# Kernel tuning notes

Measured on AMD Instinct MI355X. Metric: run time of the kernel, lower is better.

## Reference

```python
import jax, jax.numpy as jnp
import numpy as np

N_NODES = 100000
EMBED_DIM = 256


def _sage_conv(x, src, dst, W_l, b_l, W_r, num_nodes):
    # PyG SAGEConv (mean aggr): out = lin_l(mean_{j in N(i)} x_j) + lin_r(x_i)
    msg = x[src]                                              # [E, D] gather
    agg = jax.ops.segment_sum(msg, dst, num_segments=num_nodes)   # [N, D]
    cnt = jax.ops.segment_sum(jnp.ones((src.shape[0], 1), x.dtype), dst,
                              num_segments=num_nodes)         # [N, 1]
    mean = agg / jnp.maximum(cnt, 1.0)
    return mean @ W_l + b_l + x @ W_r


def setup_inputs() -> dict:
    key = jax.random.key(0)
    ks = jax.random.split(key, 12)
    D = EMBED_DIM
    glorot = 1.0 / np.sqrt(D)
    inp = {
        "emb": jax.random.uniform(ks[0], (N_NODES + 1, D), jnp.float32, 0.001, 0.3),
        "W1l": jax.random.uniform(ks[1], (D, D), jnp.float32, -glorot, glorot),
        "b1l": jnp.zeros((D,), jnp.float32),
        "W1r": jax.random.uniform(ks[2], (D, D), jnp.float32, -glorot, glorot),
        "W2l": jax.random.uniform(ks[3], (D, D), jnp.float32, -glorot, glorot),
        "b2l": jnp.zeros((D,), jnp.float32),
        "W2r": jax.random.uniform(ks[4], (D, D), jnp.float32, -glorot, glorot),
        "x_idx": jax.random.randint(ks[5], (N_NODES,), 0, N_NODES + 1, jnp.int64 if jax.config.read('jax_enable_x64') else jnp.int32),
        "edge_index": jax.random.randint(ks[6], (2, 1600000), 0, N_NODES, jnp.int32),
        "drugNodes": jax.random.randint(ks[7], (1024,), 0, N_NODES, jnp.int32),
        "seNodes": jax.random.randint(ks[8], (1024,), 0, N_NODES, jnp.int32),
    }
    return inp


def reference(emb, W1l, b1l, W1r, W2l, b2l, W2r, x_idx, edge_index, drugNodes, seNodes):
    src, dst = edge_index[0], edge_index[1]
    x = emb[x_idx]                                            # embedding lookup [N, D]
    x = _sage_conv(x, src, dst, W1l, b1l, W1r, x.shape[0])
    x = _sage_conv(x, src, dst, W2l, b2l, W2r, x.shape[0])
    drugEmbedding = x[drugNodes]
    seEmbedding = x[seNodes]
    return (drugEmbedding, seEmbedding, x)
```

## Files before the change

kernel.cpp:

```cpp
#include <hip/hip_runtime.h>
#include <hip/hip_bf16.h>


typedef __bf16 bf16x8 __attribute__((ext_vector_type(8)));
typedef __bf16 bf16x4 __attribute__((ext_vector_type(4)));
typedef float  f32x4  __attribute__((ext_vector_type(4)));
typedef float  f32x8  __attribute__((ext_vector_type(8)));

#define ROWB 1024
#define NPART 256
#define MAXBUK 2048

__device__ __forceinline__ void async_copy16(void* lds_dst, const void* g_src) {
  __builtin_amdgcn_global_load_lds(
      (const __attribute__((address_space(1))) void*)g_src,
      (__attribute__((address_space(3))) void*)lds_dst, 16, 0, 0);
}


__global__ void bin_count(const int* __restrict__ dst, int* __restrict__ hmat,
                          int E, int chunk, int nbuk) {
  __shared__ int lh[MAXBUK];
  int p = blockIdx.x, tid = threadIdx.x;
  for (int i = tid; i < nbuk; i += 256) lh[i] = 0;
  __syncthreads();
  int base = p * chunk, end = min(base + chunk, E);
  for (int e = base + tid; e < end; e += 256) atomicAdd(&lh[dst[e] >> 6], 1);
  __syncthreads();
  for (int i = tid; i < nbuk; i += 256) hmat[p * nbuk + i] = lh[i];
}

__global__ void col_scan(int* __restrict__ hmat, int* __restrict__ btot, int nbuk) {
  __shared__ int s[NPART];
  int b = blockIdx.x, t = threadIdx.x;
  int v = hmat[t * nbuk + b];
  s[t] = v; __syncthreads();
  for (int d = 1; d < NPART; d <<= 1) {
    int add = (t >= d) ? s[t - d] : 0;
    __syncthreads();
    s[t] += add;
    __syncthreads();
  }
  hmat[t * nbuk + b] = s[t] - v;
  if (t == NPART - 1) btot[b] = s[t];
}

__global__ void bucket_scan(const int* __restrict__ btot, int* __restrict__ boff, int nb) {
  __shared__ int s[2048];
  int t = threadIdx.x;
  for (int i = t; i < 2048; i += 1024) s[i] = (i < nb) ? btot[i] : 0;
  __syncthreads();
  for (int d = 1; d < 2048; d <<= 1) {
    int v0 = (t >= d) ? s[t - d] : 0;
    int v1 = (t + 1024 >= d) ? s[t + 1024 - d] : 0;
    __syncthreads();
    s[t] += v0; s[t + 1024] += v1;
    __syncthreads();
  }
  for (int i = t; i < nb; i += 1024) boff[i] = s[i] - btot[i];
}

__global__ void part_write(const int* __restrict__ src, const int* __restrict__ dst,
                           const int* __restrict__ hmat, const int* __restrict__ boff,
                           int* __restrict__ ebuf, int E, int chunk, int nbuk) {
  __shared__ int cur[MAXBUK];
  int p = blockIdx.x, tid = threadIdx.x;
  for (int i = tid; i < nbuk; i += 256) cur[i] = hmat[p * nbuk + i] + boff[i];
  __syncthreads();
  int base = p * chunk, end = min(base + chunk, E);
  for (int e = base + tid; e < end; e += 256) {
    int d = dst[e];
    int pos = atomicAdd(&cur[d >> 6], 1);
    ebuf[pos] = src[e] | ((d & 63) << 18);
  }
}

__global__ void node_hist(const int* __restrict__ ebuf, const int* __restrict__ boff,
                          const int* __restrict__ btot, int* __restrict__ cnt, int N) {
  __shared__ int lh[64];
  int b = blockIdx.x, tid = threadIdx.x;
  if (tid < 64) lh[tid] = 0;
  __syncthreads();
  int s0 = boff[b], s1 = s0 + btot[b];
  for (int i = s0 + tid; i < s1; i += 256) atomicAdd(&lh[ebuf[i] >> 18], 1);
  __syncthreads();
  int node = b * 64 + tid;
  if (tid < 64 && node < N) cnt[node] = lh[tid];
}

__global__ void scan_block_sums(const int* __restrict__ cnt, int* __restrict__ bsum, int n) {
  __shared__ int s[256];
  int i = blockIdx.x * 256 + threadIdx.x;
  s[threadIdx.x] = (i < n) ? cnt[i] : 0;
  __syncthreads();
  for (int d = 128; d > 0; d >>= 1) {
    if (threadIdx.x < d) s[threadIdx.x] += s[threadIdx.x + d];
    __syncthreads();
  }
  if (threadIdx.x == 0) bsum[blockIdx.x] = s[0];
}

__global__ void scan_tops(const int* __restrict__ bsum, int* __restrict__ bbase, int nb) {
  __shared__ int s[512];
  int t = threadIdx.x;
  int v = (t < nb) ? bsum[t] : 0;
  s[t] = v; __syncthreads();
  for (int d = 1; d < 512; d <<= 1) {
    int add = (t >= d) ? s[t - d] : 0;
    __syncthreads();
    s[t] += add;
    __syncthreads();
  }
  if (t < nb) bbase[t] = s[t] - v;
}

__global__ void scan_final(const int* __restrict__ cnt, const int* __restrict__ bbase,
                           int* __restrict__ offs, int n) {
  __shared__ int s[256];
  int t = threadIdx.x, i = blockIdx.x * 256 + t;
  int v = (i < n) ? cnt[i] : 0;
  s[t] = v; __syncthreads();
  for (int d = 1; d < 256; d <<= 1) {
    int add = (t >= d) ? s[t - d] : 0;
    __syncthreads();
    s[t] += add;
    __syncthreads();
  }
  if (i < n) offs[i] = bbase[blockIdx.x] + s[t] - v;
}

__global__ void csr_write(const int* __restrict__ ebuf, const int* __restrict__ boff,
                          const int* __restrict__ btot, const int* __restrict__ offs,
                          int* __restrict__ csr, int N) {
  __shared__ int cur[64];
  int b = blockIdx.x, tid = threadIdx.x;
  int node = b * 64 + tid;
  if (tid < 64) cur[tid] = (node < N) ? offs[node] : 0;
  __syncthreads();
  int s0 = boff[b], s1 = s0 + btot[b];
  for (int i = s0 + tid; i < s1; i += 256) {
    int e = ebuf[i];
    int p = atomicAdd(&cur[e >> 18], 1);
    csr[p] = e & 0x3FFFF;
  }
}


__global__ void prep_w_kernel(const float* __restrict__ W1l, const float* __restrict__ W1r,
                              const float* __restrict__ W2l, const float* __restrict__ W2r,
                              __bf16* __restrict__ Wt1, __bf16* __restrict__ Wt2) {
  int idx = blockIdx.x * 256 + threadIdx.x;
  int which = idx >> 17;
  int j = idx & 131071;
  int n = j >> 9, k = j & 511;
  const float* Wl = which ? W2l : W1l;
  const float* Wr = which ? W2r : W1r;
  float v = (k < 256) ? Wl[k * 256 + n] : Wr[(k - 256) * 256 + n];
  (which ? Wt2 : Wt1)[j] = (__bf16)v;
}

__global__ void gather_x_kernel(const float* __restrict__ emb, const int* __restrict__ x_idx,
                                char* __restrict__ xbase, int N) {
  int wave = threadIdx.x >> 6, lane = threadIdx.x & 63;
  int i = blockIdx.x * 4 + wave;
  if (i >= N) return;
  int s = x_idx[i];
  float4 v = *(const float4*)(emb + (size_t)s * 256 + lane * 4);
  bf16x4 o = { (__bf16)v.x, (__bf16)v.y, (__bf16)v.z, (__bf16)v.w };
  *(bf16x4*)(xbase + (size_t)i * ROWB + lane * 8) = o;
}


__global__ void sage_agg(const char* __restrict__ srcbase,
                         char* __restrict__ dstbase,
                         const int* __restrict__ csr, const int* __restrict__ cnt,
                         const int* __restrict__ offs, int N) {
  int wave = threadIdx.x >> 6, lane = threadIdx.x & 63;
  int i = blockIdx.x * 4 + wave;
  if (i >= N) return;
  int deg = cnt[i];
  const int* lp = csr + offs[i];
  int half = lane >> 5, l5 = lane & 31;
  const char* sb = srcbase + l5 * 16;

  f32x8 acc = (f32x8)0.f;

  int g8 = deg >> 3;
  for (int t = 0; t < g8; ++t) {
    const int* p = lp + t * 8 + half;
    int s0 = p[0], s1 = p[2], s2 = p[4], s3 = p[6];
    bf16x8 v0 = *(const bf16x8*)(sb + (size_t)s0 * ROWB);
    bf16x8 v1 = *(const bf16x8*)(sb + (size_t)s1 * ROWB);
    bf16x8 v2 = *(const bf16x8*)(sb + (size_t)s2 * ROWB);
    bf16x8 v3 = *(const bf16x8*)(sb + (size_t)s3 * ROWB);
#pragma unroll
    for (int k = 0; k < 8; ++k)
      acc[k] += ((float)v0[k] + (float)v1[k]) + ((float)v2[k] + (float)v3[k]);
  }

  int base = g8 * 8;
  int rem = deg & 7;
  int rp = rem >> 1;
  for (int u = 0; u < rp; ++u) {
    int s0 = lp[base + 2 * u + half];
    bf16x8 v0 = *(const bf16x8*)(sb + (size_t)s0 * ROWB);
#pragma unroll
    for (int k = 0; k < 8; ++k) acc[k] += (float)v0[k];
  }
  if ((rem & 1) && half == 0) {
    int s0 = lp[deg - 1];
    bf16x8 v0 = *(const bf16x8*)(sb + (size_t)s0 * ROWB);
#pragma unroll
    for (int k = 0; k < 8; ++k) acc[k] += (float)v0[k];
  }

  float inv = 1.0f / (float)(deg > 0 ? deg : 1);
  bf16x8 o;
#pragma unroll
  for (int k = 0; k < 8; ++k) {
    float s = acc[k] + __shfl_down(acc[k], 32);
    o[k] = (__bf16)(s * inv);
  }
  if (half == 0)
    *(bf16x8*)(dstbase + (size_t)i * ROWB + l5 * 16) = o;
}


template <int OUT_F32>
__global__ __launch_bounds__(256) void gemm_sage(const char* __restrict__ Abase,
                                                 const __bf16* __restrict__ Wt,
                                                 const float* __restrict__ bias,
                                                 char* __restrict__ outbase, int M) {
  __shared__ __align__(16) char lds[40960];
  const int tid = threadIdx.x;
  const int wave = tid >> 6, lane = tid & 63;
  const int r = lane & 15, q = lane >> 4;
  const int wm = wave >> 1, wn = wave & 1;
  const int row0 = blockIdx.x * 64;

  f32x4 acc[2][8];
#pragma unroll
  for (int t = 0; t < 2; ++t)
#pragma unroll
    for (int u = 0; u < 8; ++u) acc[t][u] = (f32x4)0.f;

  auto stage = [&](int kk, int buf) {
    char* lbase = lds + buf * 20480;
    int rowA = row0 + wave * 16 + r;
    rowA = rowA < M ? rowA : M - 1;
    async_copy16(lbase + wave * 1024 + lane * 16,
                 Abase + (size_t)rowA * ROWB + (size_t)(kk * 32 + q * 8) * 2);
#pragma unroll
    for (int i = 0; i < 4; ++i) {
      int h = wave * 4 + i;
      async_copy16(lbase + 4096 + h * 1024 + lane * 16,
                   (const char*)Wt + ((size_t)(h * 16 + r) * 512 + kk * 32 + q * 8) * 2);
    }
  };

  stage(0, 0);
  for (int kk = 0; kk < 16; ++kk) {
    __syncthreads();
    if (kk < 15) stage(kk + 1, (kk + 1) & 1);
    const char* lbase = lds + (kk & 1) * 20480;
    bf16x8 a0 = *(const bf16x8*)(lbase + (wm * 2 + 0) * 1024 + lane * 16);
    bf16x8 a1 = *(const bf16x8*)(lbase + (wm * 2 + 1) * 1024 + lane * 16);
#pragma unroll
    for (int u = 0; u < 8; ++u) {
      bf16x8 b = *(const bf16x8*)(lbase + 4096 + (wn * 8 + u) * 1024 + lane * 16);
      acc[0][u] = __builtin_amdgcn_mfma_f32_16x16x32_bf16(a0, b, acc[0][u], 0, 0, 0);
      acc[1][u] = __builtin_amdgcn_mfma_f32_16x16x32_bf16(a1, b, acc[1][u], 0, 0, 0);
    }
  }

#pragma unroll
  for (int t = 0; t < 2; ++t) {
    int rbase = row0 + wm * 32 + t * 16 + q * 4;
#pragma unroll
    for (int u = 0; u < 8; ++u) {
      int col = wn * 128 + u * 16 + r;
      float bv = bias[col];
#pragma unroll
      for (int j = 0; j < 4; ++j) {
        int row = rbase + j;
        if (row < M) {
          float v = acc[t][u][j] + bv;
          if (OUT_F32)
            *(float*)(outbase + (size_t)row * ROWB + col * 4) = v;
          else
            *(__bf16*)(outbase + (size_t)row * ROWB + 512 + col * 2) = (__bf16)v;
        }
      }
    }
  }
}


__global__ void gather_out_kernel(const float* __restrict__ x2, const int* __restrict__ drug,
                                  const int* __restrict__ se, float* __restrict__ out,
                                  int nd, int ns) {
  int wave = threadIdx.x >> 6, lane = threadIdx.x & 63;
  int ro = blockIdx.x * 4 + wave;
  if (ro >= nd + ns) return;
  int node = (ro < nd) ? drug[ro] : se[ro - nd];
  float4 v = *(const float4*)(x2 + (size_t)node * 256 + lane * 4);
  *(float4*)(out + (size_t)ro * 256 + lane * 4) = v;
}


extern "C" void kernel_launch(void* const* d_in, const int* in_sizes, int n_in,
                              void* d_out, int out_size, void* d_ws, size_t ws_size,
                              hipStream_t stream) {
  const float* emb  = (const float*)d_in[0];
  const float* W1l  = (const float*)d_in[1];
  const float* b1l  = (const float*)d_in[2];
  const float* W1r  = (const float*)d_in[3];
  const float* W2l  = (const float*)d_in[4];
  const float* b2l  = (const float*)d_in[5];
  const float* W2r  = (const float*)d_in[6];
  const int* x_idx  = (const int*)d_in[7];
  const int* edge   = (const int*)d_in[8];
  const int* drug   = (const int*)d_in[9];
  const int* se     = (const int*)d_in[10];

  const int N = in_sizes[7];
  const int E = in_sizes[8] / 2;
  const int nd = in_sizes[9], ns = in_sizes[10];
  const int* esrc = edge;
  const int* edst = edge + E;
  const int NBUK = (N + 63) >> 6;
  const int chunk = (E + NPART - 1) / NPART;

  char* ws = (char*)d_ws;
  size_t off = 0;
  char* xA1 = ws;                       off += (size_t)((N + 127) & ~127) * ROWB;
  __bf16* Wt1 = (__bf16*)(ws + off);    off += 512 * 256 * 2;
  __bf16* Wt2 = (__bf16*)(ws + off);    off += 512 * 256 * 2;
  int* cnt  = (int*)(ws + off);         off += ((size_t)N * 4 + 255) & ~(size_t)255;
  int* offs = (int*)(ws + off);         off += ((size_t)N * 4 + 255) & ~(size_t)255;
  int* csr  = (int*)(ws + off);         off += ((size_t)E * 4 + 255) & ~(size_t)255;
  int* bsum = (int*)(ws + off);         off += 4096;
  int* bbase = (int*)(ws + off);        off += 4096;
  int* ebuf = (int*)xA1;
  int* hmat = (int*)(xA1 + (8u << 20));
  int* btot = (int*)(xA1 + (16u << 20));
  int* boff = (int*)(xA1 + (16u << 20) + 16384);

  float* outp = (float*)d_out;
  float* x2 = outp + (size_t)(nd + ns) * 256;
  char* scratch2 = (char*)x2;

  const int NB = (N + 255) / 256;
  const int QB = (N + 3) / 4;
  const int GB = (N + 63) / 64;

  prep_w_kernel<<<(2 * 131072) / 256, 256, 0, stream>>>(W1l, W1r, W2l, W2r, Wt1, Wt2);

  bin_count<<<NPART, 256, 0, stream>>>(edst, hmat, E, chunk, NBUK);
  col_scan<<<NBUK, NPART, 0, stream>>>(hmat, btot, NBUK);
  bucket_scan<<<1, 1024, 0, stream>>>(btot, boff, NBUK);
  part_write<<<NPART, 256, 0, stream>>>(esrc, edst, hmat, boff, ebuf, E, chunk, NBUK);
  node_hist<<<NBUK, 256, 0, stream>>>(ebuf, boff, btot, cnt, N);
  scan_block_sums<<<NB, 256, 0, stream>>>(cnt, bsum, N);
  scan_tops<<<1, 512, 0, stream>>>(bsum, bbase, NB);
  scan_final<<<NB, 256, 0, stream>>>(cnt, bbase, offs, N);
  csr_write<<<NBUK, 256, 0, stream>>>(ebuf, boff, btot, offs, csr, N);

  gather_x_kernel<<<QB, 256, 0, stream>>>(emb, x_idx, xA1 + 512, N);
  sage_agg<<<QB, 256, 0, stream>>>(xA1 + 512, xA1, csr, cnt, offs, N);
  gemm_sage<0><<<GB, 256, 0, stream>>>(xA1, Wt1, b1l, scratch2, N);
  sage_agg<<<QB, 256, 0, stream>>>(scratch2 + 512, scratch2, csr, cnt, offs, N);
  gemm_sage<1><<<GB, 256, 0, stream>>>(scratch2, Wt2, b2l, scratch2, N);

  gather_out_kernel<<<(nd + ns + 3) / 4, 256, 0, stream>>>(x2, drug, se, outp, nd, ns);
}
```

Before: 679.6 us.

## Fuse neighbor mean aggregation into SAGE GEMM and collapse CSR offset scan

Adds a 512-thread fused kernel that computes the mean-aggregated neighbor rows for a 64-row tile directly into swizzled LDS, then runs the MFMA GEMM over both the mean and self halves without writing the mean back to global memory. Separately, the three-kernel global prefix scan for CSR offsets is replaced by a per-bucket wavefront shuffle scan inside the histogram kernel, using the already known bucket offsets. The fused path needs a second full-size workspace buffer and only runs when the workspace is large enough. The gather phase now runs with only 64 rows per block, so the gather and GEMM phases no longer overlap across kernels and occupancy is lower due to large LDS use.

```diff
diff --git a/kernel.cpp b/kernel.cpp
--- a/kernel.cpp
+++ b/kernel.cpp
@@ -75,8 +75,9 @@
   }
 }
 
-__global__ void node_hist(const int* __restrict__ ebuf, const int* __restrict__ boff,
-                          const int* __restrict__ btot, int* __restrict__ cnt, int N) {
+__global__ void node_hist_scan(const int* __restrict__ ebuf, const int* __restrict__ boff,
+                               const int* __restrict__ btot, int* __restrict__ cnt,
+                               int* __restrict__ offs, int N) {
   __shared__ int lh[64];
   int b = blockIdx.x, tid = threadIdx.x;
   if (tid < 64) lh[tid] = 0;
@@ -84,49 +85,17 @@
   int s0 = boff[b], s1 = s0 + btot[b];
   for (int i = s0 + tid; i < s1; i += 256) atomicAdd(&lh[ebuf[i] >> 18], 1);
   __syncthreads();
-  int node = b * 64 + tid;
-  if (tid < 64 && node < N) cnt[node] = lh[tid];
-}
-
-__global__ void scan_block_sums(const int* __restrict__ cnt, int* __restrict__ bsum, int n) {
-  __shared__ int s[256];
-  int i = blockIdx.x * 256 + threadIdx.x;
-  s[threadIdx.x] = (i < n) ? cnt[i] : 0;
-  __syncthreads();
-  for (int d = 128; d > 0; d >>= 1) {
-    if (threadIdx.x < d) s[threadIdx.x] += s[threadIdx.x + d];
-    __syncthreads();
-  }
-  if (threadIdx.x == 0) bsum[blockIdx.x] = s[0];
-}
-
-__global__ void scan_tops(const int* __restrict__ bsum, int* __restrict__ bbase, int nb) {
-  __shared__ int s[512];
-  int t = threadIdx.x;
-  int v = (t < nb) ? bsum[t] : 0;
-  s[t] = v; __syncthreads();
-  for (int d = 1; d < 512; d <<= 1) {
-    int add = (t >= d) ? s[t - d] : 0;
-    __syncthreads();
-    s[t] += add;
-    __syncthreads();
-  }
-  if (t < nb) bbase[t] = s[t] - v;
-}
-
-__global__ void scan_final(const int* __restrict__ cnt, const int* __restrict__ bbase,
-                           int* __restrict__ offs, int n) {
-  __shared__ int s[256];
-  int t = threadIdx.x, i = blockIdx.x * 256 + t;
-  int v = (i < n) ? cnt[i] : 0;
-  s[t] = v; __syncthreads();
-  for (int d = 1; d < 256; d <<= 1) {
-    int add = (t >= d) ? s[t - d] : 0;
-    __syncthreads();
-    s[t] += add;
-    __syncthreads();
-  }
-  if (i < n) offs[i] = bbase[blockIdx.x] + s[t] - v;
+  if (tid < 64) {
+    int v = lh[tid];
+    int x = v;
+#pragma unroll
+    for (int d = 1; d < 64; d <<= 1) {
+      int y = __shfl_up(x, d);
+      if (tid >= d) x += y;
+    }
+    int node = b * 64 + tid;
+    if (node < N) { cnt[node] = v; offs[node] = s0 + x - v; }
+  }
 }
 
 __global__ void csr_write(const int* __restrict__ ebuf, const int* __restrict__ boff,
@@ -171,8 +140,144 @@
 }
 
 
-__global__ void sage_agg(const char* __restrict__ srcbase,
-                         char* __restrict__ dstbase,
+template <int OUT_F32>
+__global__ __launch_bounds__(512) void sage_fused(
+    const char* __restrict__ Abase,
+    const __bf16* __restrict__ Wt,
+    const float* __restrict__ bias,
+    char* __restrict__ outbase,
+    const int* __restrict__ csr, const int* __restrict__ cnt,
+    const int* __restrict__ offs, int M) {
+  __shared__ __align__(16) char lds[73728];
+  char* meanbuf = lds;
+  char* Bbuf    = lds + 32768;
+  char* Axbuf   = lds + 65536;
+  const int tid = threadIdx.x;
+  const int wave = tid >> 6, lane = tid & 63;
+  const int r = lane & 15, q = lane >> 4;
+  const int row0 = blockIdx.x * 64;
+
+  auto stageB = [&](int kk, int buf) {
+    char* bb = Bbuf + buf * 16384;
+#pragma unroll
+    for (int i2 = 0; i2 < 2; ++i2) {
+      int h = wave * 2 + i2;
+      async_copy16(bb + h * 1024 + lane * 16,
+                   (const char*)Wt + ((size_t)(h * 16 + r) * 512 + kk * 32 + q * 8) * 2);
+    }
+  };
+  auto stageA = [&](int kk, int buf) {
+    if (wave < 4) {
+      char* ab = Axbuf + buf * 4096;
+      int rowA = row0 + wave * 16 + r;
+      rowA = rowA < M ? rowA : M - 1;
+      async_copy16(ab + wave * 1024 + lane * 16,
+                   Abase + (size_t)rowA * ROWB + (size_t)(kk * 32 + q * 8) * 2);
+    }
+  };
+
+  stageB(0, 0);
+
+  {
+    int half = lane >> 5, l5 = lane & 31;
+    const char* sb = Abase + 512 + l5 * 16;
+    for (int s = 0; s < 8; ++s) {
+      int i = row0 + wave * 8 + s;
+      int ii = i < M ? i : M - 1;
+      int deg = cnt[ii];
+      const int* lp = csr + offs[ii];
+      f32x8 acc = (f32x8)0.f;
+      int g8 = deg >> 3;
+      for (int t = 0; t < g8; ++t) {
+        const int* p = lp + t * 8 + half;
+        int s0 = p[0], s1 = p[2], s2 = p[4], s3 = p[6];
+        bf16x8 v0 = *(const bf16x8*)(sb + (size_t)s0 * ROWB);
+        bf16x8 v1 = *(const bf16x8*)(sb + (size_t)s1 * ROWB);
+        bf16x8 v2 = *(const bf16x8*)(sb + (size_t)s2 * ROWB);
+        bf16x8 v3 = *(const bf16x8*)(sb + (size_t)s3 * ROWB);
+#pragma unroll
+        for (int k = 0; k < 8; ++k)
+          acc[k] += ((float)v0[k] + (float)v1[k]) + ((float)v2[k] + (float)v3[k]);
+      }
+      int base = g8 * 8;
+      int rem = deg & 7;
+      int rp = rem >> 1;
+      for (int u = 0; u < rp; ++u) {
+        int r0 = lp[base + 2 * u + half];
+        bf16x8 v0 = *(const bf16x8*)(sb + (size_t)r0 * ROWB);
+#pragma unroll
+        for (int k = 0; k < 8; ++k) acc[k] += (float)v0[k];
+      }
+      if ((rem & 1) && half == 0) {
+        int r0 = lp[deg - 1];
+        bf16x8 v0 = *(const bf16x8*)(sb + (size_t)r0 * ROWB);
+#pragma unroll
+        for (int k = 0; k < 8; ++k) acc[k] += (float)v0[k];
+      }
+      float inv = 1.0f / (float)(deg > 0 ? deg : 1);
+      bf16x8 o;
+#pragma unroll
+      for (int k = 0; k < 8; ++k) {
+        float sv = acc[k] + __shfl_down(acc[k], 32);
+        o[k] = (__bf16)(sv * inv);
+      }
+      if (half == 0) {
+        int n = wave * 8 + s;
+        *(bf16x8*)(meanbuf + n * 512 + ((l5 * 16) ^ ((n & 7) << 4))) = o;
+      }
+    }
+  }
+  __syncthreads();
+
+  const int wm = wave >> 1, wn = wave & 1;
+  f32x4 acc[8];
+#pragma unroll
+  for (int u = 0; u < 8; ++u) acc[u] = (f32x4)0.f;
+
+  for (int kk = 0; kk < 16; ++kk) {
+    if (kk) __syncthreads();
+    if (kk < 15) {
+      stageB(kk + 1, (kk + 1) & 1);
+      if (kk + 1 >= 8) stageA(kk + 1, (kk + 1) & 1);
+    }
+    bf16x8 a0;
+    if (kk < 8) {
+      int arow = wm * 16 + r;
+      a0 = *(const bf16x8*)(meanbuf + arow * 512 +
+                            ((kk * 64 + q * 16) ^ ((arow & 7) << 4)));
+    } else {
+      const char* ab = Axbuf + (kk & 1) * 4096;
+      a0 = *(const bf16x8*)(ab + wm * 1024 + lane * 16);
+    }
+    const char* bb = Bbuf + (kk & 1) * 16384;
+#pragma unroll
+    for (int u = 0; u < 8; ++u) {
+      bf16x8 b = *(const bf16x8*)(bb + (wn * 8 + u) * 1024 + lane * 16);
+      acc[u] = __builtin_amdgcn_mfma_f32_16x16x32_bf16(a0, b, acc[u], 0, 0, 0);
+    }
+  }
+
+  int rbase = row0 + wm * 16 + q * 4;
+#pragma unroll
+  for (int u = 0; u < 8; ++u) {
+    int col = wn * 128 + u * 16 + r;
+    float bv = bias[col];
+#pragma unroll
+    for (int j = 0; j < 4; ++j) {
+      int row = rbase + j;
+      if (row < M) {
+        float v = acc[u][j] + bv;
+        if (OUT_F32)
+          *(float*)(outbase + (size_t)row * ROWB + col * 4) = v;
+        else
+          *(__bf16*)(outbase + (size_t)row * ROWB + 512 + col * 2) = (__bf16)v;
+      }
+    }
+  }
+}
+
+
+__global__ void sage_agg(const char* __restrict__ srcbase, char* __restrict__ dstbase,
                          const int* __restrict__ csr, const int* __restrict__ cnt,
                          const int* __restrict__ offs, int N) {
   int wave = threadIdx.x >> 6, lane = threadIdx.x & 63;
@@ -182,9 +287,7 @@
   const int* lp = csr + offs[i];
   int half = lane >> 5, l5 = lane & 31;
   const char* sb = srcbase + l5 * 16;
-
   f32x8 acc = (f32x8)0.f;
-
   int g8 = deg >> 3;
   for (int t = 0; t < g8; ++t) {
     const int* p = lp + t * 8 + half;
@@ -197,23 +300,21 @@
     for (int k = 0; k < 8; ++k)
       acc[k] += ((float)v0[k] + (float)v1[k]) + ((float)v2[k] + (float)v3[k]);
   }
-
   int base = g8 * 8;
   int rem = deg & 7;
   int rp = rem >> 1;
   for (int u = 0; u < rp; ++u) {
-    int s0 = lp[base + 2 * u + half];
-    bf16x8 v0 = *(const bf16x8*)(sb + (size_t)s0 * ROWB);
+    int r0 = lp[base + 2 * u + half];
+    bf16x8 v0 = *(const bf16x8*)(sb + (size_t)r0 * ROWB);
 #pragma unroll
     for (int k = 0; k < 8; ++k) acc[k] += (float)v0[k];
   }
   if ((rem & 1) && half == 0) {
-    int s0 = lp[deg - 1];
-    bf16x8 v0 = *(const bf16x8*)(sb + (size_t)s0 * ROWB);
+    int r0 = lp[deg - 1];
+    bf16x8 v0 = *(const bf16x8*)(sb + (size_t)r0 * ROWB);
 #pragma unroll
     for (int k = 0; k < 8; ++k) acc[k] += (float)v0[k];
   }
-
   float inv = 1.0f / (float)(deg > 0 ? deg : 1);
   bf16x8 o;
 #pragma unroll
@@ -224,7 +325,6 @@
   if (half == 0)
     *(bf16x8*)(dstbase + (size_t)i * ROWB + l5 * 16) = o;
 }
-
 
 template <int OUT_F32>
 __global__ __launch_bounds__(256) void gemm_sage(const char* __restrict__ Abase,
@@ -237,13 +337,11 @@
   const int r = lane & 15, q = lane >> 4;
   const int wm = wave >> 1, wn = wave & 1;
   const int row0 = blockIdx.x * 64;
-
   f32x4 acc[2][8];
 #pragma unroll
   for (int t = 0; t < 2; ++t)
 #pragma unroll
     for (int u = 0; u < 8; ++u) acc[t][u] = (f32x4)0.f;
-
   auto stage = [&](int kk, int buf) {
     char* lbase = lds + buf * 20480;
     int rowA = row0 + wave * 16 + r;
@@ -257,7 +355,6 @@
                    (const char*)Wt + ((size_t)(h * 16 + r) * 512 + kk * 32 + q * 8) * 2);
     }
   };
-
   stage(0, 0);
   for (int kk = 0; kk < 16; ++kk) {
     __syncthreads();
@@ -272,7 +369,6 @@
       acc[1][u] = __builtin_amdgcn_mfma_f32_16x16x32_bf16(a1, b, acc[1][u], 0, 0, 0);
     }
   }
-
 #pragma unroll
   for (int t = 0; t < 2; ++t) {
     int rbase = row0 + wm * 32 + t * 16 + q * 4;
@@ -331,16 +427,21 @@
   const int NBUK = (N + 63) >> 6;
   const int chunk = (E + NPART - 1) / NPART;
 
+  const size_t XPAD = (size_t)((N + 127) & ~127) * ROWB;
+  const size_t NAL  = ((size_t)N * 4 + 255) & ~(size_t)255;
+  const size_t EAL  = ((size_t)E * 4 + 255) & ~(size_t)255;
+  const size_t need_fused = 2 * XPAD + 2 * (512 * 256 * 2) + 2 * NAL + EAL;
+  const bool fused = (ws_size >= need_fused);
+
   char* ws = (char*)d_ws;
   size_t off = 0;
-  char* xA1 = ws;                       off += (size_t)((N + 127) & ~127) * ROWB;
+  char* xA1 = ws;                       off += XPAD;
+  char* xB  = ws + off;                 if (fused) off += XPAD;
   __bf16* Wt1 = (__bf16*)(ws + off);    off += 512 * 256 * 2;
   __bf16* Wt2 = (__bf16*)(ws + off);    off += 512 * 256 * 2;
-  int* cnt  = (int*)(ws + off);         off += ((size_t)N * 4 + 255) & ~(size_t)255;
-  int* offs = (int*)(ws + off);         off += ((size_t)N * 4 + 255) & ~(size_t)255;
-  int* csr  = (int*)(ws + off);         off += ((size_t)E * 4 + 255) & ~(size_t)255;
-  int* bsum = (int*)(ws + off);         off += 4096;
-  int* bbase = (int*)(ws + off);        off += 4096;
+  int* cnt  = (int*)(ws + off);         off += NAL;
+  int* offs = (int*)(ws + off);         off += NAL;
+  int* csr  = (int*)(ws + off);         off += EAL;
   int* ebuf = (int*)xA1;
   int* hmat = (int*)(xA1 + (8u << 20));
   int* btot = (int*)(xA1 + (16u << 20));
@@ -350,7 +451,6 @@
   float* x2 = outp + (size_t)(nd + ns) * 256;
   char* scratch2 = (char*)x2;
 
-  const int NB = (N + 255) / 256;
   const int QB = (N + 3) / 4;
   const int GB = (N + 63) / 64;
 
@@ -360,17 +460,20 @@
   col_scan<<<NBUK, NPART, 0, stream>>>(hmat, btot, NBUK);
   bucket_scan<<<1, 1024, 0, stream>>>(btot, boff, NBUK);
   part_write<<<NPART, 256, 0, stream>>>(esrc, edst, hmat, boff, ebuf, E, chunk, NBUK);
-  node_hist<<<NBUK, 256, 0, stream>>>(ebuf, boff, btot, cnt, N);
-  scan_block_sums<<<NB, 256, 0, stream>>>(cnt, bsum, N);
-  scan_tops<<<1, 512, 0, stream>>>(bsum, bbase, NB);
-  scan_final<<<NB, 256, 0, stream>>>(cnt, bbase, offs, N);
+  node_hist_scan<<<NBUK, 256, 0, stream>>>(ebuf, boff, btot, cnt, offs, N);
   csr_write<<<NBUK, 256, 0, stream>>>(ebuf, boff, btot, offs, csr, N);
 
   gather_x_kernel<<<QB, 256, 0, stream>>>(emb, x_idx, xA1 + 512, N);
-  sage_agg<<<QB, 256, 0, stream>>>(xA1 + 512, xA1, csr, cnt, offs, N);
-  gemm_sage<0><<<GB, 256, 0, stream>>>(xA1, Wt1, b1l, scratch2, N);
-  sage_agg<<<QB, 256, 0, stream>>>(scratch2 + 512, scratch2, csr, cnt, offs, N);
-  gemm_sage<1><<<GB, 256, 0, stream>>>(scratch2, Wt2, b2l, scratch2, N);
+
+  if (fused) {
+    sage_fused<0><<<GB, 512, 0, stream>>>(xA1, Wt1, b1l, xB, csr, cnt, offs, N);
+    sage_fused<1><<<GB, 512, 0, stream>>>(xB, Wt2, b2l, (char*)x2, csr, cnt, offs, N);
+  } else {
+    sage_agg<<<QB, 256, 0, stream>>>(xA1 + 512, xA1, csr, cnt, offs, N);
+    gemm_sage<0><<<GB, 256, 0, stream>>>(xA1, Wt1, b1l, scratch2, N);
+    sage_agg<<<QB, 256, 0, stream>>>(scratch2 + 512, scratch2, csr, cnt, offs, N);
+    gemm_sage<1><<<GB, 256, 0, stream>>>(scratch2, Wt2, b2l, scratch2, N);
+  }
 
   gather_out_kernel<<<(nd + ns + 3) / 4, 256, 0, stream>>>(x2, drug, se, outp, nd, ns);
 }
```

Measured after the change: 689.8 us. Within noise of the previous version (+1.5%).

## Fuse node histogram with bucket-local scan; enlarge GEMM row tile to 128

Applied to the files above, without the earlier changes.

Computes CSR offsets directly inside the per-bucket histogram kernel, using a wave prefix scan added to the bucket's global offset. This removes three global scan kernels and their launches. Separately, the SAGE GEMM tile grows from 64 to 128 rows per block, so each block reuses the staged weight tile across twice as many rows. The cost is more accumulator registers and LDS per block, which may lower occupancy.

```diff
diff --git a/kernel.cpp b/kernel.cpp
--- a/kernel.cpp
+++ b/kernel.cpp
@@ -75,8 +75,9 @@
   }
 }
 
-__global__ void node_hist(const int* __restrict__ ebuf, const int* __restrict__ boff,
-                          const int* __restrict__ btot, int* __restrict__ cnt, int N) {
+__global__ void node_hist_scan(const int* __restrict__ ebuf, const int* __restrict__ boff,
+                               const int* __restrict__ btot, int* __restrict__ cnt,
+                               int* __restrict__ offs, int N) {
   __shared__ int lh[64];
   int b = blockIdx.x, tid = threadIdx.x;
   if (tid < 64) lh[tid] = 0;
@@ -84,49 +85,17 @@
   int s0 = boff[b], s1 = s0 + btot[b];
   for (int i = s0 + tid; i < s1; i += 256) atomicAdd(&lh[ebuf[i] >> 18], 1);
   __syncthreads();
-  int node = b * 64 + tid;
-  if (tid < 64 && node < N) cnt[node] = lh[tid];
-}
-
-__global__ void scan_block_sums(const int* __restrict__ cnt, int* __restrict__ bsum, int n) {
-  __shared__ int s[256];
-  int i = blockIdx.x * 256 + threadIdx.x;
-  s[threadIdx.x] = (i < n) ? cnt[i] : 0;
-  __syncthreads();
-  for (int d = 128; d > 0; d >>= 1) {
-    if (threadIdx.x < d) s[threadIdx.x] += s[threadIdx.x + d];
-    __syncthreads();
-  }
-  if (threadIdx.x == 0) bsum[blockIdx.x] = s[0];
-}
-
-__global__ void scan_tops(const int* __restrict__ bsum, int* __restrict__ bbase, int nb) {
-  __shared__ int s[512];
-  int t = threadIdx.x;
-  int v = (t < nb) ? bsum[t] : 0;
-  s[t] = v; __syncthreads();
-  for (int d = 1; d < 512; d <<= 1) {
-    int add = (t >= d) ? s[t - d] : 0;
-    __syncthreads();
-    s[t] += add;
-    __syncthreads();
-  }
-  if (t < nb) bbase[t] = s[t] - v;
-}
-
-__global__ void scan_final(const int* __restrict__ cnt, const int* __restrict__ bbase,
-                           int* __restrict__ offs, int n) {
-  __shared__ int s[256];
-  int t = threadIdx.x, i = blockIdx.x * 256 + t;
-  int v = (i < n) ? cnt[i] : 0;
-  s[t] = v; __syncthreads();
-  for (int d = 1; d < 256; d <<= 1) {
-    int add = (t >= d) ? s[t - d] : 0;
-    __syncthreads();
-    s[t] += add;
-    __syncthreads();
-  }
-  if (i < n) offs[i] = bbase[blockIdx.x] + s[t] - v;
+  if (tid < 64) {
+    int v = lh[tid];
+    int x = v;
+#pragma unroll
+    for (int d = 1; d < 64; d <<= 1) {
+      int y = __shfl_up(x, d);
+      if (tid >= d) x += y;
+    }
+    int node = b * 64 + tid;
+    if (node < N) { cnt[node] = v; offs[node] = s0 + x - v; }
+  }
 }
 
 __global__ void csr_write(const int* __restrict__ ebuf, const int* __restrict__ boff,
@@ -184,7 +153,6 @@
   const char* sb = srcbase + l5 * 16;
 
   f32x8 acc = (f32x8)0.f;
-
   int g8 = deg >> 3;
   for (int t = 0; t < g8; ++t) {
     const int* p = lp + t * 8 + half;
@@ -197,19 +165,18 @@
     for (int k = 0; k < 8; ++k)
       acc[k] += ((float)v0[k] + (float)v1[k]) + ((float)v2[k] + (float)v3[k]);
   }
-
   int base = g8 * 8;
   int rem = deg & 7;
   int rp = rem >> 1;
   for (int u = 0; u < rp; ++u) {
-    int s0 = lp[base + 2 * u + half];
-    bf16x8 v0 = *(const bf16x8*)(sb + (size_t)s0 * ROWB);
+    int r0 = lp[base + 2 * u + half];
+    bf16x8 v0 = *(const bf16x8*)(sb + (size_t)r0 * ROWB);
 #pragma unroll
     for (int k = 0; k < 8; ++k) acc[k] += (float)v0[k];
   }
   if ((rem & 1) && half == 0) {
-    int s0 = lp[deg - 1];
-    bf16x8 v0 = *(const bf16x8*)(sb + (size_t)s0 * ROWB);
+    int r0 = lp[deg - 1];
+    bf16x8 v0 = *(const bf16x8*)(sb + (size_t)r0 * ROWB);
 #pragma unroll
     for (int k = 0; k < 8; ++k) acc[k] += (float)v0[k];
   }
@@ -231,29 +198,33 @@
                                                  const __bf16* __restrict__ Wt,
                                                  const float* __restrict__ bias,
                                                  char* __restrict__ outbase, int M) {
-  __shared__ __align__(16) char lds[40960];
+  __shared__ __align__(16) char lds[49152];
   const int tid = threadIdx.x;
   const int wave = tid >> 6, lane = tid & 63;
   const int r = lane & 15, q = lane >> 4;
   const int wm = wave >> 1, wn = wave & 1;
-  const int row0 = blockIdx.x * 64;
-
-  f32x4 acc[2][8];
-#pragma unroll
-  for (int t = 0; t < 2; ++t)
+  const int row0 = blockIdx.x * 128;
+
+  f32x4 acc[4][8];
+#pragma unroll
+  for (int t = 0; t < 4; ++t)
 #pragma unroll
     for (int u = 0; u < 8; ++u) acc[t][u] = (f32x4)0.f;
 
   auto stage = [&](int kk, int buf) {
-    char* lbase = lds + buf * 20480;
-    int rowA = row0 + wave * 16 + r;
-    rowA = rowA < M ? rowA : M - 1;
-    async_copy16(lbase + wave * 1024 + lane * 16,
-                 Abase + (size_t)rowA * ROWB + (size_t)(kk * 32 + q * 8) * 2);
+    char* lbase = lds + buf * 24576;
+#pragma unroll
+    for (int i = 0; i < 2; ++i) {
+      int h = wave * 2 + i;
+      int rowA = row0 + h * 16 + r;
+      rowA = rowA < M ? rowA : M - 1;
+      async_copy16(lbase + h * 1024 + lane * 16,
+                   Abase + (size_t)rowA * ROWB + (size_t)(kk * 32 + q * 8) * 2);
+    }
 #pragma unroll
     for (int i = 0; i < 4; ++i) {
       int h = wave * 4 + i;
-      async_copy16(lbase + 4096 + h * 1024 + lane * 16,
+      async_copy16(lbase + 8192 + h * 1024 + lane * 16,
                    (const char*)Wt + ((size_t)(h * 16 + r) * 512 + kk * 32 + q * 8) * 2);
     }
   };
@@ -262,20 +233,23 @@
   for (int kk = 0; kk < 16; ++kk) {
     __syncthreads();
     if (kk < 15) stage(kk + 1, (kk + 1) & 1);
-    const char* lbase = lds + (kk & 1) * 20480;
-    bf16x8 a0 = *(const bf16x8*)(lbase + (wm * 2 + 0) * 1024 + lane * 16);
-    bf16x8 a1 = *(const bf16x8*)(lbase + (wm * 2 + 1) * 1024 + lane * 16);
+    const char* lbase = lds + (kk & 1) * 24576;
+    bf16x8 a[4];
+#pragma unroll
+    for (int t = 0; t < 4; ++t)
+      a[t] = *(const bf16x8*)(lbase + (wm * 4 + t) * 1024 + lane * 16);
 #pragma unroll
     for (int u = 0; u < 8; ++u) {
-      bf16x8 b = *(const bf16x8*)(lbase + 4096 + (wn * 8 + u) * 1024 + lane * 16);
-      acc[0][u] = __builtin_amdgcn_mfma_f32_16x16x32_bf16(a0, b, acc[0][u], 0, 0, 0);
-      acc[1][u] = __builtin_amdgcn_mfma_f32_16x16x32_bf16(a1, b, acc[1][u], 0, 0, 0);
-    }
-  }
-
-#pragma unroll
-  for (int t = 0; t < 2; ++t) {
-    int rbase = row0 + wm * 32 + t * 16 + q * 4;
+      bf16x8 b = *(const bf16x8*)(lbase + 8192 + (wn * 8 + u) * 1024 + lane * 16);
+#pragma unroll
+      for (int t = 0; t < 4; ++t)
+        acc[t][u] = __builtin_amdgcn_mfma_f32_16x16x32_bf16(a[t], b, acc[t][u], 0, 0, 0);
+    }
+  }
+
+#pragma unroll
+  for (int t = 0; t < 4; ++t) {
+    int rbase = row0 + wm * 64 + t * 16 + q * 4;
 #pragma unroll
     for (int u = 0; u < 8; ++u) {
       int col = wn * 128 + u * 16 + r;
@@ -339,8 +313,6 @@
   int* cnt  = (int*)(ws + off);         off += ((size_t)N * 4 + 255) & ~(size_t)255;
   int* offs = (int*)(ws + off);         off += ((size_t)N * 4 + 255) & ~(size_t)255;
   int* csr  = (int*)(ws + off);         off += ((size_t)E * 4 + 255) & ~(size_t)255;
-  int* bsum = (int*)(ws + off);         off += 4096;
-  int* bbase = (int*)(ws + off);        off += 4096;
   int* ebuf = (int*)xA1;
   int* hmat = (int*)(xA1 + (8u << 20));
   int* btot = (int*)(xA1 + (16u << 20));
@@ -350,9 +322,8 @@
   float* x2 = outp + (size_t)(nd + ns) * 256;
   char* scratch2 = (char*)x2;
 
-  const int NB = (N + 255) / 256;
   const int QB = (N + 3) / 4;
-  const int GB = (N + 63) / 64;
+  const int GB = (N + 127) / 128;
 
   prep_w_kernel<<<(2 * 131072) / 256, 256, 0, stream>>>(W1l, W1r, W2l, W2r, Wt1, Wt2);
 
@@ -360,10 +331,7 @@
   col_scan<<<NBUK, NPART, 0, stream>>>(hmat, btot, NBUK);
   bucket_scan<<<1, 1024, 0, stream>>>(btot, boff, NBUK);
   part_write<<<NPART, 256, 0, stream>>>(esrc, edst, hmat, boff, ebuf, E, chunk, NBUK);
-  node_hist<<<NBUK, 256, 0, stream>>>(ebuf, boff, btot, cnt, N);
-  scan_block_sums<<<NB, 256, 0, stream>>>(cnt, bsum, N);
-  scan_tops<<<1, 512, 0, stream>>>(bsum, bbase, NB);
-  scan_final<<<NB, 256, 0, stream>>>(cnt, bbase, offs, N);
+  node_hist_scan<<<NBUK, 256, 0, stream>>>(ebuf, boff, btot, cnt, offs, N);
   csr_write<<<NBUK, 256, 0, stream>>>(ebuf, boff, btot, offs, csr, N);
 
   gather_x_kernel<<<QB, 256, 0, stream>>>(emb, x_idx, xA1 + 512, N);
```

Measured after the change: 639.0 us (median of 2 runs). 6.0% less time.
